# Kernel optimization log

Hardware: AMD Instinct MI355X
Metric: run time of the kernel (lower is better)

Reference implementation:

```python
import math
import jax, jax.numpy as jnp
import numpy as np

D_MODEL = 768
N_HEADS = 12
HEAD_DIM = D_MODEL // N_HEADS
D_FF = 3072
LN_EPS = 1e-5


def _alibi_slopes(n_heads):
    def pow2(n):
        start = 2 ** (-(2 ** (-(math.log2(n) - 3))))
        return [start * start ** i for i in range(n)]
    if n_heads & (n_heads - 1) == 0:
        s = pow2(n_heads)
    else:
        c = 2 ** math.floor(math.log2(n_heads))
        s = pow2(c) + pow2(2 * c)[0::2][: n_heads - c]
    return np.asarray(s, dtype=np.float32)  # positive; negated at use site


def _ln(t, g, b):
    m = jnp.mean(t, axis=-1, keepdims=True)
    v = jnp.mean(jnp.square(t - m), axis=-1, keepdims=True)
    return (t - m) * jax.lax.rsqrt(v + LN_EPS) * g + b


def setup_inputs() -> dict:
    key = jax.random.key(0)
    ks = jax.random.split(key, 12)
    B, N = 4, 1025
    s = 0.02
    inp = {
        "x": jax.random.normal(ks[0], (B, N, D_MODEL), dtype=jnp.float32),
        "positions": jax.random.normal(ks[1], (B, N, 2), dtype=jnp.float32) * 8.0,
        "patch_sizes": jax.random.uniform(ks[2], (B,), dtype=jnp.float32, minval=0.5, maxval=2.0),
        "num_registers": 0,
        "ln1_g": jnp.ones((D_MODEL,), jnp.float32),
        "ln1_b": jnp.zeros((D_MODEL,), jnp.float32),
        "wq": jax.random.normal(ks[3], (D_MODEL, D_MODEL), jnp.float32) * s,
        "bq": jnp.zeros((D_MODEL,), jnp.float32),
        "wk": jax.random.normal(ks[4], (D_MODEL, D_MODEL), jnp.float32) * s,
        "bk": jnp.zeros((D_MODEL,), jnp.float32),
        "wv": jax.random.normal(ks[5], (D_MODEL, D_MODEL), jnp.float32) * s,
        "bv": jnp.zeros((D_MODEL,), jnp.float32),
        "wo": jax.random.normal(ks[6], (D_MODEL, D_MODEL), jnp.float32) * s,
        "bo": jnp.zeros((D_MODEL,), jnp.float32),
        "qn_g": jnp.ones((HEAD_DIM,), jnp.float32),
        "qn_b": jnp.zeros((HEAD_DIM,), jnp.float32),
        "kn_g": jnp.ones((HEAD_DIM,), jnp.float32),
        "kn_b": jnp.zeros((HEAD_DIM,), jnp.float32),
        "ln2_g": jnp.ones((D_MODEL,), jnp.float32),
        "ln2_b": jnp.zeros((D_MODEL,), jnp.float32),
        "w1": jax.random.normal(ks[7], (D_MODEL, D_FF), jnp.float32) * s,
        "b1": jnp.zeros((D_FF,), jnp.float32),
        "w2": jax.random.normal(ks[8], (D_FF, D_MODEL), jnp.float32) * s,
        "b2": jnp.zeros((D_MODEL,), jnp.float32),
    }
    return inp


def reference(x, positions, patch_sizes, num_registers,
              ln1_g, ln1_b, wq, bq, wk, bk, wv, bv, wo, bo,
              qn_g, qn_b, kn_g, kn_b, ln2_g, ln2_b, w1, b1, w2, b2):
    B, N, d = x.shape
    H, HD = N_HEADS, HEAD_DIM

    xn = _ln(x, ln1_g, ln1_b)
    q = (xn @ wq + bq).reshape(B, N, H, HD).transpose(0, 2, 1, 3)  # [B,H,N,HD]
    k = (xn @ wk + bk).reshape(B, N, H, HD).transpose(0, 2, 1, 3)
    v = (xn @ wv + bv).reshape(B, N, H, HD).transpose(0, 2, 1, 3)
    q = _ln(q, qn_g, qn_b)  # qk-norm over head_dim
    k = _ln(k, kn_g, kn_b)

    # 2-D ALiBi bias: [B,H,N,N]
    slopes = jnp.asarray(_alibi_slopes(H))  # positive
    ps = jnp.clip(patch_sizes, 1e-6)[:, None, None]
    diff = positions[:, :, None, :] - positions[:, None, :, :]  # [B,N,N,2]
    dist = jnp.sqrt(jnp.sum(jnp.square(diff), axis=-1)) / ps  # [B,N,N]
    bias = -slopes[None, :, None, None] * dist[:, None, :, :]
    idx = jnp.arange(N)
    special = (idx == 0) | ((idx >= 1) & (idx < 1 + num_registers))  # CLS + registers
    keep = (~special).astype(x.dtype)
    bias = bias * keep[None, None, :, None] * keep[None, None, None, :]

    scale = 1.0 / math.sqrt(HD)
    scores = jnp.einsum('bhqd,bhkd->bhqk', q, k) * scale + bias
    attn = jax.nn.softmax(scores, axis=-1)
    o = jnp.einsum('bhqk,bhkd->bhqd', attn, v)
    o = o.transpose(0, 2, 1, 3).reshape(B, N, d) @ wo + bo
    x = x + o

    xn2 = _ln(x, ln2_g, ln2_b)
    mlp = jax.nn.gelu(xn2 @ w1 + b1, approximate=False) @ w2 + b2
    return x + mlp
```

## Files before the change

### kernel.cpp

```cpp
#include <hip/hip_runtime.h>
#include <hip/hip_bf16.h>
#include <math.h>

typedef __attribute__((ext_vector_type(4))) float f32x4;
typedef __attribute__((ext_vector_type(8))) short short8;

#define DMODEL 768
#define NH 12
#define HD 64
#define DFF 3072
#define KVB 64
#define NSPLIT 3
#define QH 2
#define NP 1040

struct FalseC { static constexpr bool v = false; };
struct TrueC  { static constexpr bool v = true;  };

__device__ __forceinline__ short f2bf(float f) {
    union { float f; unsigned int u; } c; c.f = f;
    unsigned int r = c.u + 0x7FFFu + ((c.u >> 16) & 1u);
    return (short)(r >> 16);
}

__device__ __forceinline__ float bf2f(short s) {
    union { unsigned int u; float f; } c; c.u = ((unsigned int)(unsigned short)s) << 16;
    return c.f;
}

__device__ __forceinline__ void gload16(const void* g, void* l) {
    __builtin_amdgcn_global_load_lds((const __attribute__((address_space(1))) void*)g,
                                     (__attribute__((address_space(3))) void*)l, 16, 0, 0);
}

__device__ __forceinline__ int xcd_swz(int o, int nwg) {
    int q = nwg >> 3, r = nwg & 7, x = o & 7, i = o >> 3;
    return (x < r ? x * (q + 1) : r * (q + 1) + (x - r) * q) + i;
}

__global__ __launch_bounds__(256) void transpose_cast(const float* __restrict__ src,
                                                      short* __restrict__ dst, int K, int Nn) {
    __shared__ float tile[32][33];
    const int n0 = blockIdx.x * 32, k0 = blockIdx.y * 32;
    const int tx = threadIdx.x & 31, ty = threadIdx.x >> 5;
    #pragma unroll
    for (int i = ty; i < 32; i += 8) {
        int k = k0 + i, n = n0 + tx;
        tile[i][tx] = (k < K && n < Nn) ? src[(size_t)k * Nn + n] : 0.f;
    }
    __syncthreads();
    #pragma unroll
    for (int i = ty; i < 32; i += 8) {
        int n = n0 + i, k = k0 + tx;
        if (n < Nn && k < K) dst[(size_t)n * K + k] = f2bf(tile[tx][i]);
    }
}

__global__ void concat_bias(const float* __restrict__ bq, const float* __restrict__ bk,
                            const float* __restrict__ bv, float* __restrict__ out) {
    int i = blockIdx.x * 256 + threadIdx.x;
    if (i < 2304) out[i] = (i < 768) ? bq[i] : (i < 1536 ? bk[i - 768] : bv[i - 1536]);
}

__global__ __launch_bounds__(256) void ln_rows(const float* __restrict__ x, const float* __restrict__ g,
                                               const float* __restrict__ bb, short* __restrict__ out, int M) {
    __shared__ float red[8];
    const int row = blockIdx.x;
    const int tid = threadIdx.x;
    const float* xr = x + (size_t)row * DMODEL;
    float v[3];
    #pragma unroll
    for (int j = 0; j < 3; j++) v[j] = xr[tid + j * 256];
    float s = v[0] + v[1] + v[2];
    #pragma unroll
    for (int mk = 32; mk; mk >>= 1) s += __shfl_xor(s, mk);
    if ((tid & 63) == 0) red[tid >> 6] = s;
    __syncthreads();
    const float mean = (red[0] + red[1] + red[2] + red[3]) * (1.0f / 768.0f);
    float sq = 0.f;
    #pragma unroll
    for (int j = 0; j < 3; j++) { float d = v[j] - mean; sq += d * d; }
    #pragma unroll
    for (int mk = 32; mk; mk >>= 1) sq += __shfl_xor(sq, mk);
    if ((tid & 63) == 0) red[4 + (tid >> 6)] = sq;
    __syncthreads();
    const float var = (red[4] + red[5] + red[6] + red[7]) * (1.0f / 768.0f);
    const float rstd = rsqrtf(var + 1e-5f);
    short* orow = out + (size_t)row * DMODEL;
    #pragma unroll
    for (int j = 0; j < 3; j++) {
        int col = tid + j * 256;
        orow[col] = f2bf((v[j] - mean) * rstd * g[col] + bb[col]);
    }
}

__global__ __launch_bounds__(256) void gemm_qkv(const short* __restrict__ A, const short* __restrict__ Bt,
        const float* __restrict__ bias,
        const float* __restrict__ qg, const float* __restrict__ qb2,
        const float* __restrict__ kg, const float* __restrict__ kb2,
        short* __restrict__ Qb, short* __restrict__ Kb, short* __restrict__ Vtp,
        int M, int B, int Nseq) {
    __shared__ short As[64 * 64];
    __shared__ short Bs[128 * 64];
    const int nbx = 18, nby = (M + 63) / 64;
    const int sid = xcd_swz(blockIdx.x, nbx * nby);
    const int n0 = (sid % nbx) * 128, m0 = (sid / nbx) * 64;
    const int tid = threadIdx.x, w = tid >> 6, lane = tid & 63, g = lane >> 4, cl = lane & 15;
    const int wm = w >> 1, wn = w & 1;
    f32x4 acc[2][4];
    #pragma unroll
    for (int a = 0; a < 2; a++)
        #pragma unroll
        for (int b2 = 0; b2 < 4; b2++) acc[a][b2] = (f32x4){0.f, 0.f, 0.f, 0.f};
    for (int kk = 0; kk < 768; kk += 64) {
        #pragma unroll
        for (int c = 0; c < 1536; c += 256) {
            int ci = c + tid;
            if (ci < 512) {
                int row = ci >> 3, p = ci & 7;
                int arow = m0 + row; if (arow >= M) arow = M - 1;
                gload16(A + (size_t)arow * 768 + kk + ((p ^ (row & 7)) << 3), &As[ci * 8]);
            } else {
                int c2 = ci - 512;
                int row = c2 >> 3, p = c2 & 7;
                gload16(Bt + (size_t)(n0 + row) * 768 + kk + ((p ^ (row & 7)) << 3), &Bs[c2 * 8]);
            }
        }
        __syncthreads();
        #pragma unroll
        for (int kh = 0; kh < 2; ++kh) {
            short8 af[2], bf[4];
            #pragma unroll
            for (int mi = 0; mi < 2; mi++) {
                int ra = wm * 32 + mi * 16 + cl;
                af[mi] = *(const short8*)&As[ra * 64 + ((((kh << 2) + g) ^ (ra & 7)) << 3)];
            }
            #pragma unroll
            for (int ni = 0; ni < 4; ni++) {
                int rb = wn * 64 + ni * 16 + cl;
                bf[ni] = *(const short8*)&Bs[rb * 64 + ((((kh << 2) + g) ^ (rb & 7)) << 3)];
            }
            #pragma unroll
            for (int mi = 0; mi < 2; mi++)
                #pragma unroll
                for (int ni = 0; ni < 4; ni++)
                    acc[mi][ni] = __builtin_amdgcn_mfma_f32_16x16x32_bf16(af[mi], bf[ni], acc[mi][ni], 0, 0, 0);
        }
        __syncthreads();
    }
    const int t = n0 / 768;
    const int h = (n0 - t * 768) / 64 + wn;
    const int b0 = m0 / Nseq, bnd = (b0 + 1) * Nseq;
    float bi[4];
    #pragma unroll
    for (int ni = 0; ni < 4; ni++) bi[ni] = bias[n0 + wn * 64 + ni * 16 + cl];
    if (t < 2) {
        const float* gp = (t == 0) ? qg : kg;
        const float* bp = (t == 0) ? qb2 : kb2;
        float gv[4], bv[4];
        #pragma unroll
        for (int ni = 0; ni < 4; ni++) { gv[ni] = gp[ni * 16 + cl]; bv[ni] = bp[ni * 16 + cl]; }
        short* out = (t == 0) ? Qb : Kb;
        #pragma unroll
        for (int mi = 0; mi < 2; mi++)
            #pragma unroll
            for (int r = 0; r < 4; r++) {
                int row = m0 + wm * 32 + mi * 16 + 4 * g + r;
                float v0 = acc[mi][0][r] + bi[0];
                float v1 = acc[mi][1][r] + bi[1];
                float v2 = acc[mi][2][r] + bi[2];
                float v3 = acc[mi][3][r] + bi[3];
                float sx = v0 + v1 + v2 + v3;
                float sxx = v0 * v0 + v1 * v1 + v2 * v2 + v3 * v3;
                #pragma unroll
                for (int mk = 8; mk; mk >>= 1) { sx += __shfl_xor(sx, mk); sxx += __shfl_xor(sxx, mk); }
                float mean = sx * (1.0f / 64.0f);
                float var = sxx * (1.0f / 64.0f) - mean * mean;
                float rstd = rsqrtf(var + 1e-5f);
                if (row < M) {
                    int bb = (row >= bnd) ? b0 + 1 : b0;
                    int n = row - bb * Nseq;
                    size_t base = (((size_t)bb * NH + h) * Nseq + n) * HD + cl;
                    out[base + 0]  = f2bf(fmaf((v0 - mean) * rstd, gv[0], bv[0]));
                    out[base + 16] = f2bf(fmaf((v1 - mean) * rstd, gv[1], bv[1]));
                    out[base + 32] = f2bf(fmaf((v2 - mean) * rstd, gv[2], bv[2]));
                    out[base + 48] = f2bf(fmaf((v3 - mean) * rstd, gv[3], bv[3]));
                }
            }
    } else {
        #pragma unroll
        for (int mi = 0; mi < 2; mi++)
            #pragma unroll
            for (int r = 0; r < 4; r++) {
                int row = m0 + wm * 32 + mi * 16 + 4 * g + r;
                if (row < M) {
                    int bb = (row >= bnd) ? b0 + 1 : b0;
                    int n = row - bb * Nseq;
                    size_t vb2 = ((size_t)bb * NH + h) * HD + cl;
                    #pragma unroll
                    for (int ni = 0; ni < 4; ni++)
                        Vtp[(vb2 + ni * 16) * NP + n] = f2bf(acc[mi][ni][r] + bi[ni]);
                }
            }
    }
}

template<int EPI, int BM, int BN>
__global__ __launch_bounds__(256) void gemm_bt(const short* __restrict__ A, const short* __restrict__ Bt,
        const float* __restrict__ bias, const float* __restrict__ res, void* __restrict__ Cv,
        int M, int Nn, int K) {
    constexpr int RN = BN / 32;
    __shared__ short As[BM * 64];
    __shared__ short Bs[BN * 64];
    const int nbx = Nn / BN, nby = (M + BM - 1) / BM;
    const int sid = xcd_swz(blockIdx.x, nbx * nby);
    const int n0 = (sid % nbx) * BN, m0 = (sid / nbx) * BM;
    const int tid = threadIdx.x, w = tid >> 6, lane = tid & 63, g = lane >> 4, cl = lane & 15;
    const int wm = w >> 1, wn = w & 1;
    f32x4 acc[2][RN];
    #pragma unroll
    for (int a = 0; a < 2; a++)
        #pragma unroll
        for (int b2 = 0; b2 < RN; b2++) acc[a][b2] = (f32x4){0.f, 0.f, 0.f, 0.f};
    constexpr int CHA = BM * 8, CHT = (BM + BN) * 8;
    for (int kk = 0; kk < K; kk += 64) {
        #pragma unroll
        for (int c = 0; c < CHT; c += 256) {
            int ci = c + tid;
            if (ci < CHA) {
                int row = ci >> 3, p = ci & 7;
                int arow = m0 + row; if (arow >= M) arow = M - 1;
                gload16(A + (size_t)arow * K + kk + ((p ^ (row & 7)) << 3), &As[ci * 8]);
            } else {
                int c2 = ci - CHA;
                int row = c2 >> 3, p = c2 & 7;
                gload16(Bt + (size_t)(n0 + row) * K + kk + ((p ^ (row & 7)) << 3), &Bs[c2 * 8]);
            }
        }
        __syncthreads();
        #pragma unroll
        for (int kh = 0; kh < 2; ++kh) {
            short8 af[2], bf[RN];
            #pragma unroll
            for (int mi = 0; mi < 2; mi++) {
                int ra = wm * (BM / 2) + mi * 16 + cl;
                af[mi] = *(const short8*)&As[ra * 64 + ((((kh << 2) + g) ^ (ra & 7)) << 3)];
            }
            #pragma unroll
            for (int ni = 0; ni < RN; ni++) {
                int rb = wn * (BN / 2) + ni * 16 + cl;
                bf[ni] = *(const short8*)&Bs[rb * 64 + ((((kh << 2) + g) ^ (rb & 7)) << 3)];
            }
            #pragma unroll
            for (int mi = 0; mi < 2; mi++)
                #pragma unroll
                for (int ni = 0; ni < RN; ni++)
                    acc[mi][ni] = __builtin_amdgcn_mfma_f32_16x16x32_bf16(af[mi], bf[ni], acc[mi][ni], 0, 0, 0);
        }
        __syncthreads();
    }
    #pragma unroll
    for (int ni = 0; ni < RN; ++ni) {
        int col = n0 + wn * (BN / 2) + ni * 16 + cl;
        float bi = bias[col];
        #pragma unroll
        for (int mi = 0; mi < 2; ++mi) {
            int rb = m0 + wm * (BM / 2) + mi * 16 + 4 * g;
            #pragma unroll
            for (int r = 0; r < 4; ++r) {
                int row = rb + r;
                if (row < M) {
                    float vv = acc[mi][ni][r] + bi;
                    if (EPI == 1) {
                        vv += res[(size_t)row * Nn + col];
                        ((float*)Cv)[(size_t)row * Nn + col] = vv;
                    } else {
                        float ge = 0.5f * vv * (1.0f + erff(vv * 0.70710678118654752f));
                        ((short*)Cv)[(size_t)row * Nn + col] = f2bf(ge);
                    }
                }
            }
        }
    }
}

__global__ __launch_bounds__(256, 3) void attn_kernel(
        const short* __restrict__ Qb, const short* __restrict__ Kb, const short* __restrict__ Vt,
        const float* __restrict__ pos, const float* __restrict__ psz, const int* __restrict__ nregp,
        short* __restrict__ opart, float* __restrict__ ppart, int B, int Nn, int nwg) {
    __shared__ short Vbuf[2][QH][4096];
    __shared__ short Pl[4][QH][16][72];
    __shared__ float Rs[4][QH][16];
    const int nqt = (Nn + 63) >> 6;
    const int sid = xcd_swz(blockIdx.x, nwg);
    const int qt = sid % nqt;
    const int rem = sid / nqt;
    const int nyy = (NH / QH) * NSPLIT;
    const int yy = rem % nyy;
    const int b = rem / nyy;
    const int h0 = (yy / NSPLIT) * QH, sp = yy % NSPLIT;
    const int tid = threadIdx.x, w = tid >> 6, lane = tid & 63, g = lane >> 4, cl = lane & 15;
    const int nreg1 = 1 + nregp[0];
    const float inv_ps = 1.0f / fmaxf(psz[b], 1e-6f);
    const float sc2 = 0.125f * 1.4426950408889634f;
    const size_t bq = (size_t)b * Nn;
    const float2* __restrict__ pos2 = (const float2*)pos;
    const int q0 = qt * 64 + w * 16;

    size_t bh[QH], vb[QH];
    short8 qa[QH][2];
    float sP[QH];
    int qr = q0 + cl; if (qr > Nn - 1) qr = Nn - 1;
    const float2 qp = pos2[bq + qr];
    const float keepq = (qr < nreg1) ? 0.f : 1.f;
    #pragma unroll
    for (int hh = 0; hh < QH; hh++) {
        int h = h0 + hh;
        bh[hh] = ((size_t)b * NH + h) * (size_t)Nn;
        vb[hh] = ((size_t)b * NH + h) * (size_t)(HD * NP);
        float slope = (h < 8) ? exp2f(-(float)(h + 1)) : exp2f(-0.5f - (float)(h - 8));
        sP[hh] = slope * inv_ps * 1.4426950408889634f * keepq;
        const short* qptr = Qb + (bh[hh] + qr) * HD;
        qa[hh][0] = *(const short8*)(qptr + 8 * g);
        qa[hh][1] = *(const short8*)(qptr + 32 + 8 * g);
    }

    int qi[4];
    #pragma unroll
    for (int i = 0; i < 4; i++) qi[i] = q0 + 4 * g + i;

    f32x4 o[QH][4];
    float psum[QH] = {0.f, 0.f};
    #pragma unroll
    for (int hh = 0; hh < QH; hh++)
        #pragma unroll
        for (int c2 = 0; c2 < 4; c2++) o[hh][c2] = (f32x4){0.f, 0.f, 0.f, 0.f};

    const int ktiles = (Nn + KVB - 1) / KVB;
    const int tps = (ktiles + NSPLIT - 1) / NSPLIT;
    const int t0 = sp * tps, t1 = min(ktiles, t0 + tps);

    auto stage = [&](int buf, int kt) {
        const int kv0 = kt * KVB;
        #pragma unroll
        for (int it = 0; it < 2 * QH; ++it) {
            int idx = it * 256 + tid;
            int hh = idx >> 9, rm = idx & 511;
            int d = rm >> 3, slot = rm & 7;
            int kvs = kv0 + ((slot ^ (d & 7)) << 3);
            gload16(Vt + vb[hh] + (size_t)d * NP + kvs, &Vbuf[buf][hh][rm * 8]);
        }
    };

    stage(0, t0);
    int cur = 0;
    for (int kt = t0; kt < t1; ++kt) {
        const int kv0 = kt * KVB;
        __syncthreads();
        if (kt + 1 < t1) stage(cur ^ 1, kt + 1);

        auto qbody = [&](int qt2, auto mc, auto tc) {
            constexpr bool KMASK = decltype(mc)::v;
            constexpr bool TAIL  = decltype(tc)::v;
            const int kbase = kv0 + qt2 * 16;
            int krow = kbase + cl;
            if (TAIL) krow = min(krow, Nn - 1);
            const short* kp0 = Kb + (bh[0] + krow) * HD;
            const short* kp1 = Kb + (bh[1] + krow) * HD;
            const short8 k00 = *(const short8*)(kp0 + 8 * g);
            const short8 k01 = *(const short8*)(kp0 + 32 + 8 * g);
            const short8 k10 = *(const short8*)(kp1 + 8 * g);
            const short8 k11 = *(const short8*)(kp1 + 32 + 8 * g);
            f32x4 s0 = __builtin_amdgcn_mfma_f32_16x16x32_bf16(k00, qa[0][0], (f32x4){0.f,0.f,0.f,0.f}, 0, 0, 0);
            s0 = __builtin_amdgcn_mfma_f32_16x16x32_bf16(k01, qa[0][1], s0, 0, 0, 0);
            f32x4 s1 = __builtin_amdgcn_mfma_f32_16x16x32_bf16(k10, qa[1][0], (f32x4){0.f,0.f,0.f,0.f}, 0, 0, 0);
            s1 = __builtin_amdgcn_mfma_f32_16x16x32_bf16(k11, qa[1][1], s1, 0, 0, 0);
            const int kb4 = kbase + 4 * g;
            float p0v[4], p1v[4];
            #pragma unroll
            for (int i = 0; i < 4; i++) {
                int ki = kb4 + i;
                int kic = TAIL ? min(ki, Nn - 1) : ki;
                float2 kp2 = pos2[bq + kic];
                float dx = qp.x - kp2.x, dy = qp.y - kp2.y;
                float dist = sqrtf(fmaf(dx, dx, dy * dy));
                if (KMASK) dist *= (ki < nreg1) ? 0.f : 1.f;
                float e0 = fmaf(s0[i], sc2, -12.0f);
                e0 = fmaf(-sP[0], dist, e0);
                float p0 = exp2f(e0);
                float e1 = fmaf(s1[i], sc2, -12.0f);
                e1 = fmaf(-sP[1], dist, e1);
                float p1 = exp2f(e1);
                if (TAIL) { bool vl = ki < Nn; p0 = vl ? p0 : 0.f; p1 = vl ? p1 : 0.f; }
                psum[0] += p0; psum[1] += p1;
                p0v[i] = p0; p1v[i] = p1;
            }
            unsigned int w00, w01, w10, w11;
            asm("v_cvt_pk_bf16_f32 %0, %1, %2" : "=v"(w00) : "v"(p0v[0]), "v"(p0v[1]));
            asm("v_cvt_pk_bf16_f32 %0, %1, %2" : "=v"(w01) : "v"(p0v[2]), "v"(p0v[3]));
            asm("v_cvt_pk_bf16_f32 %0, %1, %2" : "=v"(w10) : "v"(p1v[0]), "v"(p1v[1]));
            asm("v_cvt_pk_bf16_f32 %0, %1, %2" : "=v"(w11) : "v"(p1v[2]), "v"(p1v[3]));
            *(unsigned int*)&Pl[w][0][cl][qt2 * 16 + 4 * g]     = w00;
            *(unsigned int*)&Pl[w][0][cl][qt2 * 16 + 4 * g + 2] = w01;
            *(unsigned int*)&Pl[w][1][cl][qt2 * 16 + 4 * g]     = w10;
            *(unsigned int*)&Pl[w][1][cl][qt2 * 16 + 4 * g + 2] = w11;
        };

        const bool istail = (kv0 + KVB > Nn);
        if (!istail) {
            if (kv0 < nreg1) {
                qbody(0, TrueC{}, FalseC{}); qbody(1, TrueC{}, FalseC{});
                qbody(2, TrueC{}, FalseC{}); qbody(3, TrueC{}, FalseC{});
            } else {
                qbody(0, FalseC{}, FalseC{}); qbody(1, FalseC{}, FalseC{});
                qbody(2, FalseC{}, FalseC{}); qbody(3, FalseC{}, FalseC{});
            }
        } else {
            qbody(0, FalseC{}, TrueC{}); qbody(1, FalseC{}, TrueC{});
            qbody(2, FalseC{}, TrueC{}); qbody(3, FalseC{}, TrueC{});
        }

        #pragma unroll
        for (int hh = 0; hh < QH; hh++) {
            #pragma unroll
            for (int ks = 0; ks < 2; ++ks) {
                const short8 pf = *(const short8*)&Pl[w][hh][cl][ks * 32 + 8 * g];
                #pragma unroll
                for (int c2 = 0; c2 < 4; c2++) {
                    const int d = c2 * 16 + cl;
                    const int slot = ((ks << 2) + g) ^ (cl & 7);
                    const short8 vf = *(const short8*)&Vbuf[cur][hh][d * 64 + slot * 8];
                    o[hh][c2] = __builtin_amdgcn_mfma_f32_16x16x32_bf16(pf, vf, o[hh][c2], 0, 0, 0);
                }
            }
        }
        cur ^= 1;
    }

    #pragma unroll
    for (int hh = 0; hh < QH; hh++) {
        float r = psum[hh];
        r += __shfl_xor(r, 16);
        r += __shfl_xor(r, 32);
        if (lane < 16) Rs[w][hh][lane] = r;
    }
    float4 rs0 = *(const float4*)&Rs[w][0][4 * g];
    float4 rs1 = *(const float4*)&Rs[w][1][4 * g];
    #pragma unroll
    for (int i = 0; i < 4; i++) {
        if (qi[i] < Nn) {
            #pragma unroll
            for (int hh = 0; hh < QH; hh++) {
                size_t rbase = (((size_t)sp * B + b) * NH + (h0 + hh)) * Nn + qi[i];
                #pragma unroll
                for (int c2 = 0; c2 < 4; c2++)
                    opart[rbase * HD + c2 * 16 + cl] = f2bf(o[hh][c2][i]);
                if (cl == 0) ppart[rbase] = hh ? rs1[i] : rs0[i];
            }
        }
    }
}

__global__ __launch_bounds__(256) void attn_reduce(const short* __restrict__ opart,
        const float* __restrict__ ppart, short* __restrict__ Ob, int B, int Nn) {
    const int rows = B * NH * Nn;
    const int row = blockIdx.x * 4 + (threadIdx.x >> 6);
    if (row >= rows) return;
    const int d = threadIdx.x & 63;
    const int n = row % Nn;
    const int bh = row / Nn;
    const int h = bh % NH, b = bh / NH;
    const size_t stride = (size_t)B * NH * Nn;
    float o = 0.f, p = 0.f;
    #pragma unroll
    for (int s = 0; s < NSPLIT; s++) {
        o += bf2f(opart[((size_t)s * stride + row) * HD + d]);
        p += ppart[(size_t)s * stride + row];
    }
    Ob[((size_t)b * Nn + n) * DMODEL + h * HD + d] = f2bf(o / p);
}

extern "C" void kernel_launch(void* const* d_in, const int* in_sizes, int n_in,
                              void* d_out, int out_size, void* d_ws, size_t ws_size,
                              hipStream_t stream) {
    const float* x    = (const float*)d_in[0];
    const float* pos  = (const float*)d_in[1];
    const float* psz  = (const float*)d_in[2];
    const int*   nreg = (const int*)d_in[3];
    const float* ln1g = (const float*)d_in[4];
    const float* ln1b = (const float*)d_in[5];
    const float* wq   = (const float*)d_in[6];
    const float* bq   = (const float*)d_in[7];
    const float* wk   = (const float*)d_in[8];
    const float* bk   = (const float*)d_in[9];
    const float* wv   = (const float*)d_in[10];
    const float* bv   = (const float*)d_in[11];
    const float* wo   = (const float*)d_in[12];
    const float* bo   = (const float*)d_in[13];
    const float* qng  = (const float*)d_in[14];
    const float* qnb  = (const float*)d_in[15];
    const float* kng  = (const float*)d_in[16];
    const float* knb  = (const float*)d_in[17];
    const float* ln2g = (const float*)d_in[18];
    const float* ln2b = (const float*)d_in[19];
    const float* w1   = (const float*)d_in[20];
    const float* b1   = (const float*)d_in[21];
    const float* w2   = (const float*)d_in[22];
    const float* b2   = (const float*)d_in[23];

    const int B  = in_sizes[2];
    const int Nn = in_sizes[1] / (2 * B);
    const int M  = B * Nn;

    char* ws = (char*)d_ws;
    size_t off = 0;
    auto alloc = [&](size_t bytes) -> char* {
        char* p = ws + off;
        off += (bytes + 255) & ~(size_t)255;
        return p;
    };
    short* wt_qkv   = (short*)alloc((size_t)2304 * 768 * 2);
    short* wt_o     = (short*)alloc((size_t)768 * 768 * 2);
    short* wt_1     = (short*)alloc((size_t)3072 * 768 * 2);
    short* wt_2     = (short*)alloc((size_t)768 * 3072 * 2);
    float* bias_qkv = (float*)alloc(2304 * 4);
    short* xn       = (short*)alloc((size_t)M * 768 * 2);
    short* Qb       = (short*)alloc((size_t)M * 768 * 2);
    short* Kb       = (short*)alloc((size_t)M * 768 * 2);
    short* Vt       = (short*)alloc((size_t)B * NH * HD * NP * 2 + 4096);
    short* Ob       = (short*)alloc((size_t)M * 768 * 2);
    float* x1       = (float*)alloc((size_t)M * 768 * 4);
    short* xn2      = (short*)alloc((size_t)M * 768 * 2);
    short* hmid     = (short*)alloc((size_t)M * 3072 * 2);
    float* ppart    = (float*)alloc((size_t)NSPLIT * B * NH * Nn * 4);
    short* opart    = hmid;

    dim3 blk(256);
    transpose_cast<<<dim3(24, 24), blk, 0, stream>>>(wq, wt_qkv, 768, 768);
    transpose_cast<<<dim3(24, 24), blk, 0, stream>>>(wk, wt_qkv + 768 * 768, 768, 768);
    transpose_cast<<<dim3(24, 24), blk, 0, stream>>>(wv, wt_qkv + 2 * 768 * 768, 768, 768);
    transpose_cast<<<dim3(24, 24), blk, 0, stream>>>(wo, wt_o, 768, 768);
    transpose_cast<<<dim3(96, 24), blk, 0, stream>>>(w1, wt_1, 768, 3072);
    transpose_cast<<<dim3(24, 96), blk, 0, stream>>>(w2, wt_2, 3072, 768);
    concat_bias<<<9, blk, 0, stream>>>(bq, bk, bv, bias_qkv);

    const int MB64 = (M + 63) / 64;
    ln_rows<<<M, blk, 0, stream>>>(x, ln1g, ln1b, xn, M);
    gemm_qkv<<<18 * MB64, blk, 0, stream>>>(xn, wt_qkv, bias_qkv, qng, qnb, kng, knb,
                                            Qb, Kb, Vt, M, B, Nn);
    const int nqt = (Nn + 63) / 64;
    const int anwg = nqt * (NH / QH) * NSPLIT * B;
    attn_kernel<<<anwg, blk, 0, stream>>>(Qb, Kb, Vt, pos, psz, nreg, opart, ppart, B, Nn, anwg);
    attn_reduce<<<(B * NH * Nn + 3) / 4, blk, 0, stream>>>(opart, ppart, Ob, B, Nn);
    gemm_bt<1, 64, 64><<<12 * MB64, blk, 0, stream>>>(Ob, wt_o, bo, x, x1, M, 768, 768);
    ln_rows<<<M, blk, 0, stream>>>(x1, ln2g, ln2b, xn2, M);
    gemm_bt<2, 64, 128><<<24 * MB64, blk, 0, stream>>>(xn2, wt_1, b1, nullptr, hmid, M, 3072, 768);
    gemm_bt<1, 64, 64><<<12 * MB64, blk, 0, stream>>>(hmid, wt_2, b2, x1, (float*)d_out, M, 768, 3072);
}
```

Measured before the change: 264.7 us.

## Enlarge attention query tile to 128 with 512 threads and GEMM M-tiles to 128

The attention kernel now uses 512-thread blocks covering 128 queries, so each staged V tile is shared by eight waves, and the KV split count drops from 3 to 2. Waves whose queries fall past the sequence end skip compute but still join the barriers. The GEMM kernel is generalised to BM=128, doubling per-wave M fragments to raise operand reuse and cut tile loads. The cost is higher register pressure, fewer blocks for parallelism, and idle waves on the last query tile.

```diff
diff --git a/kernel.cpp b/kernel.cpp
--- a/kernel.cpp
+++ b/kernel.cpp
@@ -10,7 +10,7 @@
 #define HD 64
 #define DFF 3072
 #define KVB 64
-#define NSPLIT 3
+#define NSPLIT 2
 #define QH 2
 #define NP 1040
 
@@ -209,7 +209,7 @@
 __global__ __launch_bounds__(256) void gemm_bt(const short* __restrict__ A, const short* __restrict__ Bt,
         const float* __restrict__ bias, const float* __restrict__ res, void* __restrict__ Cv,
         int M, int Nn, int K) {
-    constexpr int RN = BN / 32;
+    constexpr int RM = BM / 32, RN = BN / 32;
     __shared__ short As[BM * 64];
     __shared__ short Bs[BN * 64];
     const int nbx = Nn / BN, nby = (M + BM - 1) / BM;
@@ -217,9 +217,9 @@
     const int n0 = (sid % nbx) * BN, m0 = (sid / nbx) * BM;
     const int tid = threadIdx.x, w = tid >> 6, lane = tid & 63, g = lane >> 4, cl = lane & 15;
     const int wm = w >> 1, wn = w & 1;
-    f32x4 acc[2][RN];
-    #pragma unroll
-    for (int a = 0; a < 2; a++)
+    f32x4 acc[RM][RN];
+    #pragma unroll
+    for (int a = 0; a < RM; a++)
         #pragma unroll
         for (int b2 = 0; b2 < RN; b2++) acc[a][b2] = (f32x4){0.f, 0.f, 0.f, 0.f};
     constexpr int CHA = BM * 8, CHT = (BM + BN) * 8;
@@ -240,9 +240,9 @@
         __syncthreads();
         #pragma unroll
         for (int kh = 0; kh < 2; ++kh) {
-            short8 af[2], bf[RN];
-            #pragma unroll
-            for (int mi = 0; mi < 2; mi++) {
+            short8 af[RM], bf[RN];
+            #pragma unroll
+            for (int mi = 0; mi < RM; mi++) {
                 int ra = wm * (BM / 2) + mi * 16 + cl;
                 af[mi] = *(const short8*)&As[ra * 64 + ((((kh << 2) + g) ^ (ra & 7)) << 3)];
             }
@@ -252,7 +252,7 @@
                 bf[ni] = *(const short8*)&Bs[rb * 64 + ((((kh << 2) + g) ^ (rb & 7)) << 3)];
             }
             #pragma unroll
-            for (int mi = 0; mi < 2; mi++)
+            for (int mi = 0; mi < RM; mi++)
                 #pragma unroll
                 for (int ni = 0; ni < RN; ni++)
                     acc[mi][ni] = __builtin_amdgcn_mfma_f32_16x16x32_bf16(af[mi], bf[ni], acc[mi][ni], 0, 0, 0);
@@ -264,7 +264,7 @@
         int col = n0 + wn * (BN / 2) + ni * 16 + cl;
         float bi = bias[col];
         #pragma unroll
-        for (int mi = 0; mi < 2; ++mi) {
+        for (int mi = 0; mi < RM; ++mi) {
             int rb = m0 + wm * (BM / 2) + mi * 16 + 4 * g;
             #pragma unroll
             for (int r = 0; r < 4; ++r) {
@@ -284,14 +284,14 @@
     }
 }
 
-__global__ __launch_bounds__(256, 3) void attn_kernel(
+__global__ __launch_bounds__(512, 4) void attn_kernel(
         const short* __restrict__ Qb, const short* __restrict__ Kb, const short* __restrict__ Vt,
         const float* __restrict__ pos, const float* __restrict__ psz, const int* __restrict__ nregp,
         short* __restrict__ opart, float* __restrict__ ppart, int B, int Nn, int nwg) {
     __shared__ short Vbuf[2][QH][4096];
-    __shared__ short Pl[4][QH][16][72];
-    __shared__ float Rs[4][QH][16];
-    const int nqt = (Nn + 63) >> 6;
+    __shared__ short Pl[8][QH][16][68];
+    __shared__ float Rs[8][QH][16];
+    const int nqt = (Nn + 127) >> 7;
     const int sid = xcd_swz(blockIdx.x, nwg);
     const int qt = sid % nqt;
     const int rem = sid / nqt;
@@ -305,7 +305,8 @@
     const float sc2 = 0.125f * 1.4426950408889634f;
     const size_t bq = (size_t)b * Nn;
     const float2* __restrict__ pos2 = (const float2*)pos;
-    const int q0 = qt * 64 + w * 16;
+    const int q0 = qt * 128 + w * 16;
+    const bool active = q0 < Nn;
 
     size_t bh[QH], vb[QH];
     short8 qa[QH][2];
@@ -343,8 +344,8 @@
     auto stage = [&](int buf, int kt) {
         const int kv0 = kt * KVB;
         #pragma unroll
-        for (int it = 0; it < 2 * QH; ++it) {
-            int idx = it * 256 + tid;
+        for (int it = 0; it < 2; ++it) {
+            int idx = it * 512 + tid;
             int hh = idx >> 9, rm = idx & 511;
             int d = rm >> 3, slot = rm & 7;
             int kvs = kv0 + ((slot ^ (d & 7)) << 3);
@@ -359,103 +360,107 @@
         __syncthreads();
         if (kt + 1 < t1) stage(cur ^ 1, kt + 1);
 
-        auto qbody = [&](int qt2, auto mc, auto tc) {
-            constexpr bool KMASK = decltype(mc)::v;
-            constexpr bool TAIL  = decltype(tc)::v;
-            const int kbase = kv0 + qt2 * 16;
-            int krow = kbase + cl;
-            if (TAIL) krow = min(krow, Nn - 1);
-            const short* kp0 = Kb + (bh[0] + krow) * HD;
-            const short* kp1 = Kb + (bh[1] + krow) * HD;
-            const short8 k00 = *(const short8*)(kp0 + 8 * g);
-            const short8 k01 = *(const short8*)(kp0 + 32 + 8 * g);
-            const short8 k10 = *(const short8*)(kp1 + 8 * g);
-            const short8 k11 = *(const short8*)(kp1 + 32 + 8 * g);
-            f32x4 s0 = __builtin_amdgcn_mfma_f32_16x16x32_bf16(k00, qa[0][0], (f32x4){0.f,0.f,0.f,0.f}, 0, 0, 0);
-            s0 = __builtin_amdgcn_mfma_f32_16x16x32_bf16(k01, qa[0][1], s0, 0, 0, 0);
-            f32x4 s1 = __builtin_amdgcn_mfma_f32_16x16x32_bf16(k10, qa[1][0], (f32x4){0.f,0.f,0.f,0.f}, 0, 0, 0);
-            s1 = __builtin_amdgcn_mfma_f32_16x16x32_bf16(k11, qa[1][1], s1, 0, 0, 0);
-            const int kb4 = kbase + 4 * g;
-            float p0v[4], p1v[4];
-            #pragma unroll
-            for (int i = 0; i < 4; i++) {
-                int ki = kb4 + i;
-                int kic = TAIL ? min(ki, Nn - 1) : ki;
-                float2 kp2 = pos2[bq + kic];
-                float dx = qp.x - kp2.x, dy = qp.y - kp2.y;
-                float dist = sqrtf(fmaf(dx, dx, dy * dy));
-                if (KMASK) dist *= (ki < nreg1) ? 0.f : 1.f;
-                float e0 = fmaf(s0[i], sc2, -12.0f);
-                e0 = fmaf(-sP[0], dist, e0);
-                float p0 = exp2f(e0);
-                float e1 = fmaf(s1[i], sc2, -12.0f);
-                e1 = fmaf(-sP[1], dist, e1);
-                float p1 = exp2f(e1);
-                if (TAIL) { bool vl = ki < Nn; p0 = vl ? p0 : 0.f; p1 = vl ? p1 : 0.f; }
-                psum[0] += p0; psum[1] += p1;
-                p0v[i] = p0; p1v[i] = p1;
-            }
-            unsigned int w00, w01, w10, w11;
-            asm("v_cvt_pk_bf16_f32 %0, %1, %2" : "=v"(w00) : "v"(p0v[0]), "v"(p0v[1]));
-            asm("v_cvt_pk_bf16_f32 %0, %1, %2" : "=v"(w01) : "v"(p0v[2]), "v"(p0v[3]));
-            asm("v_cvt_pk_bf16_f32 %0, %1, %2" : "=v"(w10) : "v"(p1v[0]), "v"(p1v[1]));
-            asm("v_cvt_pk_bf16_f32 %0, %1, %2" : "=v"(w11) : "v"(p1v[2]), "v"(p1v[3]));
-            *(unsigned int*)&Pl[w][0][cl][qt2 * 16 + 4 * g]     = w00;
-            *(unsigned int*)&Pl[w][0][cl][qt2 * 16 + 4 * g + 2] = w01;
-            *(unsigned int*)&Pl[w][1][cl][qt2 * 16 + 4 * g]     = w10;
-            *(unsigned int*)&Pl[w][1][cl][qt2 * 16 + 4 * g + 2] = w11;
-        };
-
-        const bool istail = (kv0 + KVB > Nn);
-        if (!istail) {
-            if (kv0 < nreg1) {
-                qbody(0, TrueC{}, FalseC{}); qbody(1, TrueC{}, FalseC{});
-                qbody(2, TrueC{}, FalseC{}); qbody(3, TrueC{}, FalseC{});
+        if (active) {
+            auto qbody = [&](int qt2, auto mc, auto tc) {
+                constexpr bool KMASK = decltype(mc)::v;
+                constexpr bool TAIL  = decltype(tc)::v;
+                const int kbase = kv0 + qt2 * 16;
+                int krow = kbase + cl;
+                if (TAIL) krow = min(krow, Nn - 1);
+                const short* kp0 = Kb + (bh[0] + krow) * HD;
+                const short* kp1 = Kb + (bh[1] + krow) * HD;
+                const short8 k00 = *(const short8*)(kp0 + 8 * g);
+                const short8 k01 = *(const short8*)(kp0 + 32 + 8 * g);
+                const short8 k10 = *(const short8*)(kp1 + 8 * g);
+                const short8 k11 = *(const short8*)(kp1 + 32 + 8 * g);
+                f32x4 s0 = __builtin_amdgcn_mfma_f32_16x16x32_bf16(k00, qa[0][0], (f32x4){0.f,0.f,0.f,0.f}, 0, 0, 0);
+                s0 = __builtin_amdgcn_mfma_f32_16x16x32_bf16(k01, qa[0][1], s0, 0, 0, 0);
+                f32x4 s1 = __builtin_amdgcn_mfma_f32_16x16x32_bf16(k10, qa[1][0], (f32x4){0.f,0.f,0.f,0.f}, 0, 0, 0);
+                s1 = __builtin_amdgcn_mfma_f32_16x16x32_bf16(k11, qa[1][1], s1, 0, 0, 0);
+                const int kb4 = kbase + 4 * g;
+                float p0v[4], p1v[4];
+                #pragma unroll
+                for (int i = 0; i < 4; i++) {
+                    int ki = kb4 + i;
+                    int kic = TAIL ? min(ki, Nn - 1) : ki;
+                    float2 kp2 = pos2[bq + kic];
+                    float dx = qp.x - kp2.x, dy = qp.y - kp2.y;
+                    float dist = sqrtf(fmaf(dx, dx, dy * dy));
+                    if (KMASK) dist *= (ki < nreg1) ? 0.f : 1.f;
+                    float e0 = fmaf(s0[i], sc2, -12.0f);
+                    e0 = fmaf(-sP[0], dist, e0);
+                    float p0 = exp2f(e0);
+                    float e1 = fmaf(s1[i], sc2, -12.0f);
+                    e1 = fmaf(-sP[1], dist, e1);
+                    float p1 = exp2f(e1);
+                    if (TAIL) { bool vl = ki < Nn; p0 = vl ? p0 : 0.f; p1 = vl ? p1 : 0.f; }
+                    psum[0] += p0; psum[1] += p1;
+                    p0v[i] = p0; p1v[i] = p1;
+                }
+                unsigned int w00, w01, w10, w11;
+                asm("v_cvt_pk_bf16_f32 %0, %1, %2" : "=v"(w00) : "v"(p0v[0]), "v"(p0v[1]));
+                asm("v_cvt_pk_bf16_f32 %0, %1, %2" : "=v"(w01) : "v"(p0v[2]), "v"(p0v[3]));
+                asm("v_cvt_pk_bf16_f32 %0, %1, %2" : "=v"(w10) : "v"(p1v[0]), "v"(p1v[1]));
+                asm("v_cvt_pk_bf16_f32 %0, %1, %2" : "=v"(w11) : "v"(p1v[2]), "v"(p1v[3]));
+                *(unsigned int*)&Pl[w][0][cl][qt2 * 16 + 4 * g]     = w00;
+                *(unsigned int*)&Pl[w][0][cl][qt2 * 16 + 4 * g + 2] = w01;
+                *(unsigned int*)&Pl[w][1][cl][qt2 * 16 + 4 * g]     = w10;
+                *(unsigned int*)&Pl[w][1][cl][qt2 * 16 + 4 * g + 2] = w11;
+            };
+
+            const bool istail = (kv0 + KVB > Nn);
+            if (!istail) {
+                if (kv0 < nreg1) {
+                    qbody(0, TrueC{}, FalseC{}); qbody(1, TrueC{}, FalseC{});
+                    qbody(2, TrueC{}, FalseC{}); qbody(3, TrueC{}, FalseC{});
+                } else {
+                    qbody(0, FalseC{}, FalseC{}); qbody(1, FalseC{}, FalseC{});
+                    qbody(2, FalseC{}, FalseC{}); qbody(3, FalseC{}, FalseC{});
+                }
             } else {
-                qbody(0, FalseC{}, FalseC{}); qbody(1, FalseC{}, FalseC{});
-                qbody(2, FalseC{}, FalseC{}); qbody(3, FalseC{}, FalseC{});
-            }
-        } else {
-            qbody(0, FalseC{}, TrueC{}); qbody(1, FalseC{}, TrueC{});
-            qbody(2, FalseC{}, TrueC{}); qbody(3, FalseC{}, TrueC{});
-        }
-
+                qbody(0, FalseC{}, TrueC{}); qbody(1, FalseC{}, TrueC{});
+                qbody(2, FalseC{}, TrueC{}); qbody(3, FalseC{}, TrueC{});
+            }
+
+            #pragma unroll
+            for (int hh = 0; hh < QH; hh++) {
+                #pragma unroll
+                for (int ks = 0; ks < 2; ++ks) {
+                    const short8 pf = *(const short8*)&Pl[w][hh][cl][ks * 32 + 8 * g];
+                    #pragma unroll
+                    for (int c2 = 0; c2 < 4; c2++) {
+                        const int d = c2 * 16 + cl;
+                        const int slot = ((ks << 2) + g) ^ (cl & 7);
+                        const short8 vf = *(const short8*)&Vbuf[cur][hh][d * 64 + slot * 8];
+                        o[hh][c2] = __builtin_amdgcn_mfma_f32_16x16x32_bf16(pf, vf, o[hh][c2], 0, 0, 0);
+                    }
+                }
+            }
+        }
+        cur ^= 1;
+    }
+
+    if (active) {
         #pragma unroll
         for (int hh = 0; hh < QH; hh++) {
-            #pragma unroll
-            for (int ks = 0; ks < 2; ++ks) {
-                const short8 pf = *(const short8*)&Pl[w][hh][cl][ks * 32 + 8 * g];
+            float r = psum[hh];
+            r += __shfl_xor(r, 16);
+            r += __shfl_xor(r, 32);
+            if (lane < 16) Rs[w][hh][lane] = r;
+        }
+        float4 rs0 = *(const float4*)&Rs[w][0][4 * g];
+        float4 rs1 = *(const float4*)&Rs[w][1][4 * g];
+        #pragma unroll
+        for (int i = 0; i < 4; i++) {
+            if (qi[i] < Nn) {
                 #pragma unroll
-                for (int c2 = 0; c2 < 4; c2++) {
-                    const int d = c2 * 16 + cl;
-                    const int slot = ((ks << 2) + g) ^ (cl & 7);
-                    const short8 vf = *(const short8*)&Vbuf[cur][hh][d * 64 + slot * 8];
-                    o[hh][c2] = __builtin_amdgcn_mfma_f32_16x16x32_bf16(pf, vf, o[hh][c2], 0, 0, 0);
-                }
-            }
-        }
-        cur ^= 1;
-    }
-
-    #pragma unroll
-    for (int hh = 0; hh < QH; hh++) {
-        float r = psum[hh];
-        r += __shfl_xor(r, 16);
-        r += __shfl_xor(r, 32);
-        if (lane < 16) Rs[w][hh][lane] = r;
-    }
-    float4 rs0 = *(const float4*)&Rs[w][0][4 * g];
-    float4 rs1 = *(const float4*)&Rs[w][1][4 * g];
-    #pragma unroll
-    for (int i = 0; i < 4; i++) {
-        if (qi[i] < Nn) {
-            #pragma unroll
-            for (int hh = 0; hh < QH; hh++) {
-                size_t rbase = (((size_t)sp * B + b) * NH + (h0 + hh)) * Nn + qi[i];
-                #pragma unroll
-                for (int c2 = 0; c2 < 4; c2++)
-                    opart[rbase * HD + c2 * 16 + cl] = f2bf(o[hh][c2][i]);
-                if (cl == 0) ppart[rbase] = hh ? rs1[i] : rs0[i];
+                for (int hh = 0; hh < QH; hh++) {
+                    size_t rbase = (((size_t)sp * B + b) * NH + (h0 + hh)) * Nn + qi[i];
+                    #pragma unroll
+                    for (int c2 = 0; c2 < 4; c2++)
+                        opart[rbase * HD + c2 * 16 + cl] = f2bf(o[hh][c2][i]);
+                    if (cl == 0) ppart[rbase] = hh ? rs1[i] : rs0[i];
+                }
             }
         }
     }
@@ -545,15 +550,16 @@
     concat_bias<<<9, blk, 0, stream>>>(bq, bk, bv, bias_qkv);
 
     const int MB64 = (M + 63) / 64;
+    const int MB128 = (M + 127) / 128;
     ln_rows<<<M, blk, 0, stream>>>(x, ln1g, ln1b, xn, M);
     gemm_qkv<<<18 * MB64, blk, 0, stream>>>(xn, wt_qkv, bias_qkv, qng, qnb, kng, knb,
                                             Qb, Kb, Vt, M, B, Nn);
-    const int nqt = (Nn + 63) / 64;
+    const int nqt = (Nn + 127) / 128;
     const int anwg = nqt * (NH / QH) * NSPLIT * B;
-    attn_kernel<<<anwg, blk, 0, stream>>>(Qb, Kb, Vt, pos, psz, nreg, opart, ppart, B, Nn, anwg);
+    attn_kernel<<<anwg, dim3(512), 0, stream>>>(Qb, Kb, Vt, pos, psz, nreg, opart, ppart, B, Nn, anwg);
     attn_reduce<<<(B * NH * Nn + 3) / 4, blk, 0, stream>>>(opart, ppart, Ob, B, Nn);
-    gemm_bt<1, 64, 64><<<12 * MB64, blk, 0, stream>>>(Ob, wt_o, bo, x, x1, M, 768, 768);
+    gemm_bt<1, 128, 64><<<12 * MB128, blk, 0, stream>>>(Ob, wt_o, bo, x, x1, M, 768, 768);
     ln_rows<<<M, blk, 0, stream>>>(x1, ln2g, ln2b, xn2, M);
-    gemm_bt<2, 64, 128><<<24 * MB64, blk, 0, stream>>>(xn2, wt_1, b1, nullptr, hmid, M, 3072, 768);
-    gemm_bt<1, 64, 64><<<12 * MB64, blk, 0, stream>>>(hmid, wt_2, b2, x1, (float*)d_out, M, 768, 3072);
-}
+    gemm_bt<2, 128, 128><<<24 * MB128, blk, 0, stream>>>(xn2, wt_1, b1, nullptr, hmid, M, 3072, 768);
+    gemm_bt<1, 128, 64><<<12 * MB128, blk, 0, stream>>>(hmid, wt_2, b2, x1, (float*)d_out, M, 768, 3072);
+}
```

After: 302.6 us. 1.14x slower.
